# Kernel optimization log

Measured on AMD Instinct MI355X. Metric: run time of the kernel, lower is better.

Reference implementation:

```python
import jax, jax.numpy as jnp
import numpy as np

B, C_IN, IMG = 64, 3, 384
P = 16                 # patch size / conv stride
HID = 768              # hidden_size
CQ = HID // 8          # query/key channels in CrissCrossAttention
H = W = IMG // P       # 24x24 token grid
NP = H * W             # 576 patches
NEG_INF = -1e30        # finite stand-in for -inf diagonal mask (grad-safe)


def setup_inputs() -> dict:
    key = jax.random.key(0)
    ks = jax.random.split(key, 10)
    s = lambda fan_in: 1.0 / np.sqrt(fan_in)
    return {
        "x": jax.random.normal(ks[0], (B, C_IN, IMG, IMG), jnp.float32),
        "patch_w": jax.random.normal(ks[1], (HID, C_IN, P, P), jnp.float32) * s(C_IN * P * P),
        "patch_b": jax.random.normal(ks[2], (HID,), jnp.float32) * 0.02,
        "wq": jax.random.normal(ks[3], (CQ, HID), jnp.float32) * s(HID),
        "bq": jax.random.normal(ks[4], (CQ,), jnp.float32) * 0.02,
        "wk": jax.random.normal(ks[5], (CQ, HID), jnp.float32) * s(HID),
        "bk": jax.random.normal(ks[6], (CQ,), jnp.float32) * 0.02,
        "wv": jax.random.normal(ks[7], (HID, HID), jnp.float32) * s(HID),
        "bv": jax.random.normal(ks[8], (HID,), jnp.float32) * 0.02,
        "gamma": jnp.zeros((1,), jnp.float32),
        "pos_emb": jax.random.normal(ks[9], (1, NP, HID), jnp.float32) * 0.02,
    }


def criss_cross_attention(x, wq, bq, wk, bk, wv, bv, gamma):
    # x: [b, c, h, w]
    b, c, h, w = x.shape
    q = jnp.einsum('oc,bchw->bohw', wq, x) + bq[None, :, None, None]   # [b,cq,h,w]
    k = jnp.einsum('oc,bchw->bohw', wk, x) + bk[None, :, None, None]   # [b,cq,h,w]
    v = jnp.einsum('oc,bchw->bohw', wv, x) + bv[None, :, None, None]   # [b,c,h,w]

    # column (H-axis) attention energies with -inf on the diagonal (self-pair)
    energy_H = jnp.einsum('bciw,bcjw->biwj', q, k)                     # [b,h,w,h]
    eye = jnp.eye(h, dtype=bool)[:, None, :]                           # [h,1,h]
    energy_H = jnp.where(eye, NEG_INF, energy_H)
    # row (W-axis) attention energies
    energy_W = jnp.einsum('bchi,bchj->bhij', q, k)                     # [b,h,w,w]

    concate = jax.nn.softmax(jnp.concatenate([energy_H, energy_W], axis=3), axis=3)
    att_H = concate[..., :h]                                           # [b,h,w,h]
    att_W = concate[..., h:]                                           # [b,h,w,w]

    out_H = jnp.einsum('biwj,bcjw->bciw', att_H, v)                    # [b,c,h,w]
    out_W = jnp.einsum('bhij,bchj->bchi', att_W, v)                    # [b,c,h,w]
    return gamma[0] * (out_H + out_W) + x


def reference(x, patch_w, patch_b, wq, bq, wk, bk, wv, bv, gamma, pos_emb):
    # patch embedding: Conv2d(3->768, kernel=16, stride=16)
    y = jax.lax.conv_general_dilated(
        x, patch_w, window_strides=(P, P), padding='VALID',
        dimension_numbers=('NCHW', 'OIHW', 'NCHW'))
    y = y + patch_b[None, :, None, None]                               # [b,768,24,24]
    y = criss_cross_attention(y, wq, bq, wk, bk, wv, bv, gamma)
    y = y.reshape(y.shape[0], y.shape[1], -1).transpose(0, 2, 1)       # [b, 576, 768]
    emb = y + pos_emb                                                  # dropout: eval-mode identity
    return emb
```

## Files before the change

kernel.cpp:

```cpp
#include <hip/hip_runtime.h>
#include <hip/hip_bf16.h>
#include <cstdint>

#define BATCH 64
#define CIN 3
#define IMG 384
#define PATCH 16
#define HID 768
#define CQ 96
#define HW24 24
#define NP 576
#define MROWS (BATCH*NP)
#define KDIM 768
#define NVQK 1024
#define NT_K 12
#define NEGINF (-1e30f)

typedef __attribute__((ext_vector_type(8))) short s16x8;
typedef __attribute__((ext_vector_type(4))) float f32x4;

__device__ __forceinline__ float bf2f(unsigned short u) {
    union { unsigned int i; float f; } x; x.i = ((unsigned int)u) << 16; return x.f;
}
__device__ __forceinline__ unsigned short f2bf(float f) {
    union { float f; unsigned int i; } x; x.f = f;
    unsigned int r = x.i + 0x7fffu + ((x.i >> 16) & 1u);
    return (unsigned short)(r >> 16);
}
__device__ __forceinline__ unsigned int f2bf2(float a, float b) {
    union { __hip_bfloat162 h; unsigned int u; } c;
    c.h = __float22bfloat162_rn(make_float2(a, b));
    return c.u;
}

__device__ __forceinline__ void gload_lds16(const void* g, void* l) {
    __builtin_amdgcn_global_load_lds(
        (const __attribute__((address_space(1))) void*)(uintptr_t)g,
        (__attribute__((address_space(3))) void*)(uint32_t)(uintptr_t)l,
        16, 0, 0);
}

__device__ __forceinline__ size_t kp_addr(int row, int col) {
    return (((size_t)(row >> 8) * NT_K + (col >> 6)) * 256 + (row & 255)) * 64 + (col & 63);
}

__global__ void k_prep(const float* __restrict__ pw, const float* __restrict__ wq,
                       const float* __restrict__ wk, const float* __restrict__ wv,
                       const float* __restrict__ bq, const float* __restrict__ bk,
                       const float* __restrict__ bv,
                       unsigned short* __restrict__ Wp, unsigned short* __restrict__ Wvqk,
                       float* __restrict__ Bvqk) {
    int t = blockIdx.x * 256 + threadIdx.x;
    if (t < HID * HID) Wp[t] = f2bf(pw[t]);
    if (t < NVQK * HID) {
        int row = t / HID; int col = t - row * HID;
        float val = 0.f;
        if (row < 768) val = wv[t];
        else if (row < 864) val = wq[(row - 768) * HID + col];
        else if (row < 960) val = wk[(row - 864) * HID + col];
        Wvqk[t] = f2bf(val);
    }
    if (t < NVQK) {
        float v = 0.f;
        if (t < 768) v = bv[t]; else if (t < 864) v = bq[t - 768]; else if (t < 960) v = bk[t - 864];
        Bvqk[t] = v;
    }
}

__device__ __forceinline__ void stageB_half(const unsigned short* __restrict__ gmat,
        int growbase, char* ldsregion, int kcol, int rl, int sp, int ldsoff0) {
    const unsigned short* g0 = gmat + (size_t)(growbase + rl) * KDIM + kcol + sp * 8;
    gload_lds16(g0, ldsregion + ldsoff0);
    gload_lds16(g0 + (size_t)8 * KDIM, ldsregion + ldsoff0 + 1024);
}

__global__ __launch_bounds__(512, 2) void k_gemmFused(
    const float* __restrict__ x, const unsigned short* __restrict__ Bw,
    const float* __restrict__ bias, unsigned short* __restrict__ Y,
    float* __restrict__ outF, const float* __restrict__ pos,
    const float* __restrict__ gamma)
{
    extern __shared__ char smem[];
    const int tid  = threadIdx.x;
    const int lane = tid & 63;
    const int w    = tid >> 6;
    const int wm   = w >> 2;
    const int wn   = w & 3;

    const int nwg = gridDim.x;
    const int chunk = nwg >> 3;
    const int bid = blockIdx.x;
    const int bs = (bid & 7) * chunk + (bid >> 3);
    const int bx = bs / 3, by = bs - (bs / 3) * 3;
    const int blockN = by << 8;

    const int rl = (w << 4) + (lane >> 3);
    const int sp = (lane & 7) ^ (lane >> 3);
    const int ldsoff0 = (w << 11) + (lane << 4);

    const int lx   = (lane & 15) << 7;
    const int swz  = (lane & 7) << 4;
    const int cbx0 = (((lane >> 4) << 4)) ^ swz;
    const int cbx1 = (64 + ((lane >> 4) << 4)) ^ swz;

    const int rr  = tid >> 1;
    const int ch  = (tid & 1) << 5;
    const int iib = ch >> 4;
    const int grow = (bx << 8) + rr;
    const int b  = grow / NP;
    const int p  = grow - b * NP;
    const int ph = p / HW24, pw = p - ph * HW24;
    const float* xrow = x + (size_t)b * (CIN * IMG * IMG) + ph * (PATCH * IMG) + pw * PATCH;
    const int swzr  = (rr & 7) << 4;
    const int wbase = rr * 128;

    char* Acur = smem;
    char* Anxt = smem + 32768;
    char* Bcur = smem + 65536;
    char* Bnxt = smem + 98304;

    float4 ld[8];
    auto loadA = [&](int t) {
        const float* src = xrow + (t >> 2) * (IMG * IMG) + ((t & 3) * 4 + iib) * IMG;
        #pragma unroll
        for (int u = 0; u < 4; ++u) {
            const float* s2 = src + (u >> 1) * IMG + ((u & 1) << 3);
            ld[2 * u]     = *(const float4*)s2;
            ld[2 * u + 1] = *(const float4*)(s2 + 4);
        }
    };
    auto writeA = [&](char* dst) {
        #pragma unroll
        for (int u = 0; u < 4; ++u) {
            int4 pk;
            pk.x = f2bf2(ld[2 * u].x,     ld[2 * u].y);
            pk.y = f2bf2(ld[2 * u].z,     ld[2 * u].w);
            pk.z = f2bf2(ld[2 * u + 1].x, ld[2 * u + 1].y);
            pk.w = f2bf2(ld[2 * u + 1].z, ld[2 * u + 1].w);
            *reinterpret_cast<int4*>(dst + wbase + ((ch * 2 + u * 16) ^ swzr)) = pk;
        }
    };

    loadA(0);
    stageB_half(Bw, blockN,       Bcur,         0, rl, sp, ldsoff0);
    stageB_half(Bw, blockN + 128, Bcur + 16384, 0, rl, sp, ldsoff0);
    asm volatile("s_waitcnt vmcnt(0)" ::: "memory");
    __builtin_amdgcn_sched_barrier(0);
    writeA(Acur);
    asm volatile("s_waitcnt lgkmcnt(0)" ::: "memory");
    __builtin_amdgcn_sched_barrier(0);
    __builtin_amdgcn_s_barrier();

    f32x4 acc[8][4] = {};

    for (int t = 0; t < NT_K; ++t) {
        if (t + 1 < NT_K) {
            loadA(t + 1);
            stageB_half(Bw, blockN,       Bnxt,         (t + 1) << 6, rl, sp, ldsoff0);
            stageB_half(Bw, blockN + 128, Bnxt + 16384, (t + 1) << 6, rl, sp, ldsoff0);
        }
        s16x8 bfr[4][2];
        #pragma unroll
        for (int nf = 0; nf < 4; ++nf) {
            const int rb = wn * 8192 + nf * 2048 + lx;
            bfr[nf][0] = *(const s16x8*)(Bcur + rb + cbx0);
            bfr[nf][1] = *(const s16x8*)(Bcur + rb + cbx1);
        }
        #pragma unroll
        for (int half = 0; half < 2; ++half) {
            s16x8 af[4][2];
            #pragma unroll
            for (int m = 0; m < 4; ++m) {
                const int rb0 = wm * 16384 + (half * 4 + m) * 2048 + lx;
                af[m][0] = *(const s16x8*)(Acur + rb0 + cbx0);
                af[m][1] = *(const s16x8*)(Acur + rb0 + cbx1);
            }
            __builtin_amdgcn_s_setprio(1);
            #pragma unroll
            for (int kh = 0; kh < 2; ++kh)
                #pragma unroll
                for (int m = 0; m < 4; ++m)
                    #pragma unroll
                    for (int nf = 0; nf < 4; ++nf)
                        acc[half * 4 + m][nf] = __builtin_amdgcn_mfma_f32_16x16x32_bf16(
                            bfr[nf][kh], af[m][kh], acc[half * 4 + m][nf], 0, 0, 0);
            __builtin_amdgcn_s_setprio(0);
        }
        if (t + 1 < NT_K) {
            __builtin_amdgcn_sched_barrier(0);
            asm volatile("s_waitcnt vmcnt(0)" ::: "memory");
            __builtin_amdgcn_sched_barrier(0);
            writeA(Anxt);
            asm volatile("s_waitcnt lgkmcnt(0)" ::: "memory");
            __builtin_amdgcn_sched_barrier(0);
            __builtin_amdgcn_s_barrier();
            char* ta = Acur; Acur = Anxt; Anxt = ta;
            char* tb = Bcur; Bcur = Bnxt; Bnxt = tb;
        }
    }

    const int rowb = (bx << 8) + wm * 128 + (lane & 15);
    const int colb = blockN + wn * 64 + ((lane >> 4) << 2);
    const float g = gamma[0];
    if (g == 0.f) {
        #pragma unroll
        for (int mf = 0; mf < 8; ++mf) {
            const int row = rowb + mf * 16;
            const int px = row % NP;
            #pragma unroll
            for (int nf = 0; nf < 4; ++nf) {
                const int col = colb + nf * 16;
                float4 bs4 = *(const float4*)(bias + col);
                float4 pv  = *(const float4*)(pos + (size_t)px * HID + col);
                f32x4 a = acc[mf][nf];
                float4 o;
                o.x = a[0] + bs4.x + pv.x;
                o.y = a[1] + bs4.y + pv.y;
                o.z = a[2] + bs4.z + pv.z;
                o.w = a[3] + bs4.w + pv.w;
                *reinterpret_cast<float4*>(outF + (size_t)row * HID + col) = o;
            }
        }
    } else {
        #pragma unroll
        for (int mf = 0; mf < 8; ++mf) {
            const int row = rowb + mf * 16;
            #pragma unroll
            for (int nf = 0; nf < 4; ++nf) {
                const int col = colb + nf * 16;
                float4 bs4 = *(const float4*)(bias + col);
                f32x4 a = acc[mf][nf];
                ushort4 o;
                o.x = f2bf(a[0] + bs4.x);
                o.y = f2bf(a[1] + bs4.y);
                o.z = f2bf(a[2] + bs4.z);
                o.w = f2bf(a[3] + bs4.w);
                *reinterpret_cast<ushort4*>(Y + kp_addr(row, col)) = o;
            }
        }
    }
}

__device__ __forceinline__ void stageA_half(const unsigned short* __restrict__ Ap,
        size_t tilebase, int h, char* ldsregion, int rl, int sp, int ldsoff0) {
    const unsigned short* g0 = Ap + tilebase + (size_t)(h * 128 + rl) * 64 + sp * 8;
    gload_lds16(g0, ldsregion + ldsoff0);
    gload_lds16(g0 + 512, ldsregion + ldsoff0 + 1024);
}

__global__ __launch_bounds__(512, 2) void k_gemm256(
    const unsigned short* __restrict__ A, const unsigned short* __restrict__ Bw,
    const float* __restrict__ bias, unsigned short* __restrict__ C,
    const float* __restrict__ gamma, int NT)
{
    if (gamma[0] == 0.f) return;
    extern __shared__ char smem[];
    const int tid  = threadIdx.x;
    const int lane = tid & 63;
    const int w    = tid >> 6;
    const int wm   = w >> 2;
    const int wn   = w & 3;
    const int nwg = gridDim.x;
    const int chunk = nwg >> 3;
    const int bid = blockIdx.x;
    const int bs = (bid & 7) * chunk + (bid >> 3);
    const int bx = bs / NT, by = bs - (bs / NT) * NT;
    const int blockN = by << 8;
    const int rl = (w << 4) + (lane >> 3);
    const int sp = (lane & 7) ^ (lane >> 3);
    const int ldsoff0 = (w << 11) + (lane << 4);
    const int lx   = (lane & 15) << 7;
    const int swz  = (lane & 7) << 4;
    const int cbx0 = (((lane >> 4) << 4)) ^ swz;
    const int cbx1 = (64 + ((lane >> 4) << 4)) ^ swz;
    char* pa0 = smem;
    char* pa1 = smem + 32768;
    char* pa2 = smem + 65536;
    char* pb0 = smem + 98304;
    char* pb1 = smem + 131072;
    const size_t atile0 = ((size_t)bx * NT_K) << 14;

    stageB_half(Bw, blockN,       pb0,         0,  rl, sp, ldsoff0);
    stageB_half(Bw, blockN + 128, pb0 + 16384, 0,  rl, sp, ldsoff0);
    stageA_half(A, atile0,         0, pa0,         rl, sp, ldsoff0);
    stageA_half(A, atile0,         1, pa0 + 16384, rl, sp, ldsoff0);
    stageA_half(A, atile0 + 16384, 0, pa1,         rl, sp, ldsoff0);
    stageA_half(A, atile0 + 16384, 1, pa1 + 16384, rl, sp, ldsoff0);

    f32x4 acc[8][4] = {};
    asm volatile("s_waitcnt vmcnt(4)" ::: "memory");
    __builtin_amdgcn_sched_barrier(0);
    __builtin_amdgcn_s_barrier();

    for (int t = 0; t < NT_K; ++t) {
        if (t + 1 < NT_K) {
            stageB_half(Bw, blockN,       pb1,         (t + 1) << 6, rl, sp, ldsoff0);
            stageB_half(Bw, blockN + 128, pb1 + 16384, (t + 1) << 6, rl, sp, ldsoff0);
        }
        if (t + 2 < NT_K) {
            const size_t tb = atile0 + ((size_t)(t + 2) << 14);
            stageA_half(A, tb, 0, pa2,         rl, sp, ldsoff0);
            stageA_half(A, tb, 1, pa2 + 16384, rl, sp, ldsoff0);
        }
        s16x8 bfr[4][2];
        #pragma unroll
        for (int nf = 0; nf < 4; ++nf) {
            const int rb = wn * 8192 + nf * 2048 + lx;
            bfr[nf][0] = *(const s16x8*)(pb0 + rb + cbx0);
            bfr[nf][1] = *(const s16x8*)(pb0 + rb + cbx1);
        }
        #pragma unroll
        for (int half = 0; half < 2; ++half) {
            s16x8 af[4][2];
            #pragma unroll
            for (int m = 0; m < 4; ++m) {
                const int rb0 = wm * 16384 + (half * 4 + m) * 2048 + lx;
                af[m][0] = *(const s16x8*)(pa0 + rb0 + cbx0);
                af[m][1] = *(const s16x8*)(pa0 + rb0 + cbx1);
            }
            __builtin_amdgcn_s_setprio(1);
            #pragma unroll
            for (int kh = 0; kh < 2; ++kh)
                #pragma unroll
                for (int m = 0; m < 4; ++m)
                    #pragma unroll
                    for (int nf = 0; nf < 4; ++nf)
                        acc[half * 4 + m][nf] = __builtin_amdgcn_mfma_f32_16x16x32_bf16(
                            bfr[nf][kh], af[m][kh], acc[half * 4 + m][nf], 0, 0, 0);
            __builtin_amdgcn_s_setprio(0);
        }
        if (t < NT_K - 1) {
            __builtin_amdgcn_sched_barrier(0);
            if (t >= NT_K - 3) { asm volatile("s_waitcnt vmcnt(0)" ::: "memory"); }
            else               { asm volatile("s_waitcnt vmcnt(4)" ::: "memory"); }
            __builtin_amdgcn_s_barrier();
            __builtin_amdgcn_sched_barrier(0);
        }
        char* ta = pa0; pa0 = pa1; pa1 = pa2; pa2 = ta;
        char* tb = pb0; pb0 = pb1; pb1 = tb;
    }

    const int rowb = (bx << 8) + wm * 128 + (lane & 15);
    const int colb = blockN + wn * 64 + ((lane >> 4) << 2);
    #pragma unroll
    for (int mf = 0; mf < 8; ++mf) {
        const int row = rowb + mf * 16;
        #pragma unroll
        for (int nf = 0; nf < 4; ++nf) {
            const int col = colb + nf * 16;
            float4 bs4 = *(const float4*)(bias + col);
            f32x4 a = acc[mf][nf];
            ushort4 o;
            o.x = f2bf(a[0] + bs4.x);
            o.y = f2bf(a[1] + bs4.y);
            o.z = f2bf(a[2] + bs4.z);
            o.w = f2bf(a[3] + bs4.w);
            *reinterpret_cast<ushort4*>(C + (size_t)row * (NT << 8) + col) = o;
        }
    }
}

__global__ __launch_bounds__(256) void k_energyH(const unsigned short* __restrict__ VQK,
                                                 float* __restrict__ E, const float* __restrict__ gam) {
    if (gam[0] == 0.f) return;
    __shared__ float qs[24][97], ks[24][97];
    const int b = blockIdx.x / HW24, w = blockIdx.x % HW24;
    const int tid = threadIdx.x;
    for (int idx = tid; idx < 24 * 12; idx += 256) {
        int i = idx / 12, c = (idx % 12) * 8;
        size_t base = ((size_t)(b * NP + i * HW24 + w)) * NVQK + 768;
        s16x8 qv = *(const s16x8*)(VQK + base + c);
        s16x8 kv = *(const s16x8*)(VQK + base + 96 + c);
        #pragma unroll
        for (int u = 0; u < 8; u++) {
            qs[i][c + u] = bf2f((unsigned short)qv[u]);
            ks[i][c + u] = bf2f((unsigned short)kv[u]);
        }
    }
    __syncthreads();
    for (int idx = tid; idx < 576; idx += 256) {
        int i = idx / 24, j = idx - (idx / 24) * 24;
        float s = NEGINF;
        if (i != j) {
            s = 0.f;
            #pragma unroll 8
            for (int c = 0; c < 96; c++) s += qs[i][c] * ks[j][c];
        }
        E[((size_t)(b * NP + i * HW24 + w)) * 48 + j] = s;
    }
}

__global__ __launch_bounds__(256) void k_energyW(const unsigned short* __restrict__ VQK,
                                                 float* __restrict__ E, const float* __restrict__ gam) {
    if (gam[0] == 0.f) return;
    __shared__ float qs[24][97], ks[24][97], ew[24][24];
    const int b = blockIdx.x / HW24, h = blockIdx.x % HW24;
    const int tid = threadIdx.x;
    const int prow = b * NP + h * HW24;
    for (int idx = tid; idx < 24 * 12; idx += 256) {
        int i = idx / 12, c = (idx % 12) * 8;
        size_t base = ((size_t)(prow + i)) * NVQK + 768;
        s16x8 qv = *(const s16x8*)(VQK + base + c);
        s16x8 kv = *(const s16x8*)(VQK + base + 96 + c);
        #pragma unroll
        for (int u = 0; u < 8; u++) {
            qs[i][c + u] = bf2f((unsigned short)qv[u]);
            ks[i][c + u] = bf2f((unsigned short)kv[u]);
        }
    }
    __syncthreads();
    for (int idx = tid; idx < 576; idx += 256) {
        int i = idx / 24, j = idx - (idx / 24) * 24;
        float s = 0.f;
        #pragma unroll 8
        for (int c = 0; c < 96; c++) s += qs[i][c] * ks[j][c];
        ew[i][j] = s;
    }
    __syncthreads();
    if (tid < 24) {
        size_t p = prow + tid;
        float e[48];
        #pragma unroll
        for (int j = 0; j < 24; j++) e[j] = E[p * 48 + j];
        #pragma unroll
        for (int j = 0; j < 24; j++) e[24 + j] = ew[tid][j];
        float mx = NEGINF;
        #pragma unroll
        for (int j = 0; j < 48; j++) mx = fmaxf(mx, e[j]);
        float sum = 0.f;
        #pragma unroll
        for (int j = 0; j < 48; j++) { e[j] = __expf(e[j] - mx); sum += e[j]; }
        float inv = 1.f / sum;
        #pragma unroll
        for (int j = 0; j < 48; j++) E[p * 48 + j] = e[j] * inv;
    }
}

__global__ __launch_bounds__(192) void k_passH(const float* __restrict__ E,
        const unsigned short* __restrict__ VQK, const unsigned short* __restrict__ Y,
        const float* __restrict__ gamma, const float* __restrict__ pos,
        float* __restrict__ out) {
    const float g = gamma[0];
    if (g == 0.f) return;
    __shared__ float att[576];
    int bid = (blockIdx.x & 7) * 192 + (blockIdx.x >> 3);
    const int b = bid / HW24, w = bid % HW24;
    const int tid = threadIdx.x;
    for (int idx = tid; idx < 576; idx += 192) {
        int i = idx / 24, j = idx - (idx / 24) * 24;
        att[idx] = E[((size_t)(b * NP + i * HW24 + w)) * 48 + j];
    }
    __syncthreads();
    float vf[24][4];
    #pragma unroll
    for (int j = 0; j < 24; j++) {
        ushort4 vv = *(const ushort4*)(VQK + ((size_t)(b * NP + j * HW24 + w)) * NVQK + 4 * tid);
        vf[j][0] = bf2f(vv.x); vf[j][1] = bf2f(vv.y); vf[j][2] = bf2f(vv.z); vf[j][3] = bf2f(vv.w);
    }
    #pragma unroll
    for (int i = 0; i < 24; i++) {
        float a0 = 0.f, a1 = 0.f, a2 = 0.f, a3 = 0.f;
        #pragma unroll
        for (int j = 0; j < 24; j++) {
            float a = att[i * 24 + j];
            a0 += a * vf[j][0]; a1 += a * vf[j][1]; a2 += a * vf[j][2]; a3 += a * vf[j][3];
        }
        size_t p = (size_t)(b * NP + i * HW24 + w);
        ushort4 yv = *(const ushort4*)(Y + kp_addr((int)p, 4 * tid));
        float4 pv = *(const float4*)(pos + (size_t)(i * HW24 + w) * HID + 4 * tid);
        float4 o;
        o.x = g * a0 + bf2f(yv.x) + pv.x;
        o.y = g * a1 + bf2f(yv.y) + pv.y;
        o.z = g * a2 + bf2f(yv.z) + pv.z;
        o.w = g * a3 + bf2f(yv.w) + pv.w;
        *reinterpret_cast<float4*>(out + p * HID + 4 * tid) = o;
    }
}

__global__ __launch_bounds__(192) void k_passW(const float* __restrict__ E,
        const unsigned short* __restrict__ VQK, const float* __restrict__ gamma,
        float* __restrict__ out) {
    const float g = gamma[0];
    if (g == 0.f) return;
    __shared__ float att[576];
    int bid = (blockIdx.x & 7) * 192 + (blockIdx.x >> 3);
    const int b = bid / HW24, h = bid % HW24;
    const int tid = threadIdx.x;
    const int prow = b * NP + h * HW24;
    for (int idx = tid; idx < 576; idx += 192) {
        int i = idx / 24, j = idx - (idx / 24) * 24;
        att[idx] = E[((size_t)(prow + i)) * 48 + 24 + j];
    }
    __syncthreads();
    float vf[24][4];
    #pragma unroll
    for (int j = 0; j < 24; j++) {
        ushort4 vv = *(const ushort4*)(VQK + ((size_t)(prow + j)) * NVQK + 4 * tid);
        vf[j][0] = bf2f(vv.x); vf[j][1] = bf2f(vv.y); vf[j][2] = bf2f(vv.z); vf[j][3] = bf2f(vv.w);
    }
    #pragma unroll
    for (int i = 0; i < 24; i++) {
        float a0 = 0.f, a1 = 0.f, a2 = 0.f, a3 = 0.f;
        #pragma unroll
        for (int j = 0; j < 24; j++) {
            float a = att[i * 24 + j];
            a0 += a * vf[j][0]; a1 += a * vf[j][1]; a2 += a * vf[j][2]; a3 += a * vf[j][3];
        }
        size_t p = (size_t)(prow + i);
        float4 o = *reinterpret_cast<const float4*>(out + p * HID + 4 * tid);
        o.x += g * a0; o.y += g * a1; o.z += g * a2; o.w += g * a3;
        *reinterpret_cast<float4*>(out + p * HID + 4 * tid) = o;
    }
}

extern "C" void kernel_launch(void* const* d_in, const int* in_sizes, int n_in,
                              void* d_out, int out_size, void* d_ws, size_t ws_size,
                              hipStream_t stream) {
    const float* x       = (const float*)d_in[0];
    const float* patch_w = (const float*)d_in[1];
    const float* patch_b = (const float*)d_in[2];
    const float* wq      = (const float*)d_in[3];
    const float* bq      = (const float*)d_in[4];
    const float* wk      = (const float*)d_in[5];
    const float* bk      = (const float*)d_in[6];
    const float* wv      = (const float*)d_in[7];
    const float* bv      = (const float*)d_in[8];
    const float* gamma   = (const float*)d_in[9];
    const float* pos_emb = (const float*)d_in[10];
    float* out = (float*)d_out;

    hipFuncSetAttribute(reinterpret_cast<const void*>(k_gemmFused),
                        hipFuncAttributeMaxDynamicSharedMemorySize, 131072);
    hipFuncSetAttribute(reinterpret_cast<const void*>(k_gemm256),
                        hipFuncAttributeMaxDynamicSharedMemorySize, 163840);

    char* ws = (char*)d_ws;
    size_t off = 0;
    auto alloc = [&](size_t bytes) { char* pp = ws + off; off += (bytes + 255) & ~(size_t)255; return pp; };
    unsigned short* VQK = (unsigned short*)alloc((size_t)MROWS * NVQK * 2);
    unsigned short* Y   = (unsigned short*)alloc((size_t)MROWS * HID * 2);
    unsigned short* Wp  = (unsigned short*)alloc((size_t)HID * HID * 2);
    unsigned short* Wvqk= (unsigned short*)alloc((size_t)NVQK * HID * 2);
    float*          Bvqk= (float*)alloc(NVQK * 4);
    float*          E   = (float*)alloc((size_t)MROWS * 48 * 4);

    k_prep<<<dim3((NVQK * HID + 255) / 256), dim3(256), 0, stream>>>(patch_w, wq, wk, wv, bq, bk, bv, Wp, Wvqk, Bvqk);
    k_gemmFused<<<dim3((MROWS / 256) * (HID / 256)), dim3(512), 131072, stream>>>(
        x, Wp, patch_b, Y, out, pos_emb, gamma);
    k_gemm256<<<dim3((MROWS / 256) * (NVQK / 256)), dim3(512), 163840, stream>>>(
        Y, Wvqk, Bvqk, VQK, gamma, NVQK / 256);
    k_energyH<<<dim3(BATCH * HW24), dim3(256), 0, stream>>>(VQK, E, gamma);
    k_energyW<<<dim3(BATCH * HW24), dim3(256), 0, stream>>>(VQK, E, gamma);
    k_passH<<<dim3(BATCH * HW24), dim3(192), 0, stream>>>(E, VQK, Y, gamma, pos_emb, out);
    k_passW<<<dim3(BATCH * HW24), dim3(192), 0, stream>>>(E, VQK, gamma, out);
}
```

Baseline: 112.0 us.

## Deepen patch-embed GEMM pipeline to prefetch two K-tiles ahead

Converts the fused patch-embedding GEMM from double buffering to a three-stage B buffer and two register sets for A. Loads for tile t+2 are issued while tile t computes, with partial vmcnt waits, so global-memory latency is hidden further. The cost is 160KB of LDS and launch bounds lowered to one block per CU, which halves occupancy and puts more pressure on registers.

```diff
diff --git a/kernel.cpp b/kernel.cpp
--- a/kernel.cpp
+++ b/kernel.cpp
@@ -74,7 +74,7 @@
     gload_lds16(g0 + (size_t)8 * KDIM, ldsregion + ldsoff0 + 1024);
 }
 
-__global__ __launch_bounds__(512, 2) void k_gemmFused(
+__global__ __launch_bounds__(512, 1) void k_gemmFused(
     const float* __restrict__ x, const unsigned short* __restrict__ Bw,
     const float* __restrict__ bias, unsigned short* __restrict__ Y,
     float* __restrict__ outF, const float* __restrict__ pos,
@@ -114,13 +114,15 @@
     const int swzr  = (rr & 7) << 4;
     const int wbase = rr * 128;
 
-    char* Acur = smem;
-    char* Anxt = smem + 32768;
-    char* Bcur = smem + 65536;
-    char* Bnxt = smem + 98304;
-
-    float4 ld[8];
-    auto loadA = [&](int t) {
+    char* paC = smem;
+    char* paN = smem + 32768;
+    char* pb0 = smem + 65536;
+    char* pb1 = smem + 98304;
+    char* pb2 = smem + 131072;
+
+    float4 ld0[8], ld1[8];
+
+    auto loadA = [&](int t, float4 (&ld)[8]) {
         const float* src = xrow + (t >> 2) * (IMG * IMG) + ((t & 3) * 4 + iib) * IMG;
         #pragma unroll
         for (int u = 0; u < 4; ++u) {
@@ -129,7 +131,7 @@
             ld[2 * u + 1] = *(const float4*)(s2 + 4);
         }
     };
-    auto writeA = [&](char* dst) {
+    auto writeA = [&](char* dst, float4 (&ld)[8]) {
         #pragma unroll
         for (int u = 0; u < 4; ++u) {
             int4 pk;
@@ -141,30 +143,35 @@
         }
     };
 
-    loadA(0);
-    stageB_half(Bw, blockN,       Bcur,         0, rl, sp, ldsoff0);
-    stageB_half(Bw, blockN + 128, Bcur + 16384, 0, rl, sp, ldsoff0);
-    asm volatile("s_waitcnt vmcnt(0)" ::: "memory");
+    f32x4 acc[8][4] = {};
+
+    loadA(0, ld0);
+    stageB_half(Bw, blockN,       pb0,         0, rl, sp, ldsoff0);
+    stageB_half(Bw, blockN + 128, pb0 + 16384, 0, rl, sp, ldsoff0);
+    loadA(1, ld1);
+    stageB_half(Bw, blockN,       pb1,         64, rl, sp, ldsoff0);
+    stageB_half(Bw, blockN + 128, pb1 + 16384, 64, rl, sp, ldsoff0);
+    asm volatile("s_waitcnt vmcnt(16)" ::: "memory");
     __builtin_amdgcn_sched_barrier(0);
-    writeA(Acur);
+    writeA(paC, ld0);
+    asm volatile("s_waitcnt vmcnt(12)" ::: "memory");
     asm volatile("s_waitcnt lgkmcnt(0)" ::: "memory");
     __builtin_amdgcn_sched_barrier(0);
     __builtin_amdgcn_s_barrier();
 
-    f32x4 acc[8][4] = {};
-
-    for (int t = 0; t < NT_K; ++t) {
-        if (t + 1 < NT_K) {
-            loadA(t + 1);
-            stageB_half(Bw, blockN,       Bnxt,         (t + 1) << 6, rl, sp, ldsoff0);
-            stageB_half(Bw, blockN + 128, Bnxt + 16384, (t + 1) << 6, rl, sp, ldsoff0);
+    auto tileBody = [&](int t, float4 (&ldIss)[8], float4 (&ldWr)[8]) {
+        const bool issue = (t + 2 < NT_K);
+        if (issue) {
+            loadA(t + 2, ldIss);
+            stageB_half(Bw, blockN,       pb2,         (t + 2) << 6, rl, sp, ldsoff0);
+            stageB_half(Bw, blockN + 128, pb2 + 16384, (t + 2) << 6, rl, sp, ldsoff0);
         }
         s16x8 bfr[4][2];
         #pragma unroll
         for (int nf = 0; nf < 4; ++nf) {
             const int rb = wn * 8192 + nf * 2048 + lx;
-            bfr[nf][0] = *(const s16x8*)(Bcur + rb + cbx0);
-            bfr[nf][1] = *(const s16x8*)(Bcur + rb + cbx1);
+            bfr[nf][0] = *(const s16x8*)(pb0 + rb + cbx0);
+            bfr[nf][1] = *(const s16x8*)(pb0 + rb + cbx1);
         }
         #pragma unroll
         for (int half = 0; half < 2; ++half) {
@@ -172,8 +179,8 @@
             #pragma unroll
             for (int m = 0; m < 4; ++m) {
                 const int rb0 = wm * 16384 + (half * 4 + m) * 2048 + lx;
-                af[m][0] = *(const s16x8*)(Acur + rb0 + cbx0);
-                af[m][1] = *(const s16x8*)(Acur + rb0 + cbx1);
+                af[m][0] = *(const s16x8*)(paC + rb0 + cbx0);
+                af[m][1] = *(const s16x8*)(paC + rb0 + cbx1);
             }
             __builtin_amdgcn_s_setprio(1);
             #pragma unroll
@@ -186,17 +193,24 @@
                             bfr[nf][kh], af[m][kh], acc[half * 4 + m][nf], 0, 0, 0);
             __builtin_amdgcn_s_setprio(0);
         }
-        if (t + 1 < NT_K) {
+        if (t < NT_K - 1) {
             __builtin_amdgcn_sched_barrier(0);
-            asm volatile("s_waitcnt vmcnt(0)" ::: "memory");
+            if (issue) { asm volatile("s_waitcnt vmcnt(12)" ::: "memory"); }
+            else       { asm volatile("s_waitcnt vmcnt(0)"  ::: "memory"); }
             __builtin_amdgcn_sched_barrier(0);
-            writeA(Anxt);
+            writeA(paN, ldWr);
             asm volatile("s_waitcnt lgkmcnt(0)" ::: "memory");
             __builtin_amdgcn_sched_barrier(0);
             __builtin_amdgcn_s_barrier();
-            char* ta = Acur; Acur = Anxt; Anxt = ta;
-            char* tb = Bcur; Bcur = Bnxt; Bnxt = tb;
-        }
+            char* ta = paC; paC = paN; paN = ta;
+            char* tb = pb0; pb0 = pb1; pb1 = pb2; pb2 = tb;
+        }
+    };
+
+    #pragma unroll 1
+    for (int tt = 0; tt < NT_K; tt += 2) {
+        tileBody(tt,     ld0, ld1);
+        tileBody(tt + 1, ld1, ld0);
     }
 
     const int rowb = (bx << 8) + wm * 128 + (lane & 15);
@@ -530,7 +544,7 @@
     float* out = (float*)d_out;
 
     hipFuncSetAttribute(reinterpret_cast<const void*>(k_gemmFused),
-                        hipFuncAttributeMaxDynamicSharedMemorySize, 131072);
+                        hipFuncAttributeMaxDynamicSharedMemorySize, 163840);
     hipFuncSetAttribute(reinterpret_cast<const void*>(k_gemm256),
                         hipFuncAttributeMaxDynamicSharedMemorySize, 163840);
 
@@ -545,7 +559,7 @@
     float*          E   = (float*)alloc((size_t)MROWS * 48 * 4);
 
     k_prep<<<dim3((NVQK * HID + 255) / 256), dim3(256), 0, stream>>>(patch_w, wq, wk, wv, bq, bk, bv, Wp, Wvqk, Bvqk);
-    k_gemmFused<<<dim3((MROWS / 256) * (HID / 256)), dim3(512), 131072, stream>>>(
+    k_gemmFused<<<dim3((MROWS / 256) * (HID / 256)), dim3(512), 163840, stream>>>(
         x, Wp, patch_b, Y, out, pos_emb, gamma);
     k_gemm256<<<dim3((MROWS / 256) * (NVQK / 256)), dim3(512), 163840, stream>>>(
         Y, Wvqk, Bvqk, VQK, gamma, NVQK / 256);
```

New measurement: 319.8 us. 2.86x slower.

## Retile patch-embed GEMM to 128x384 blocks with narrower im2col loads

Applied to the files above, without the earlier changes.

The fused patch-embedding GEMM moves from 256x256 output tiles (3 N-blocks) to 128x384 tiles (2 N-blocks). Each warp now computes a 64x96 sub-tile, so every A fragment is reused across six B fragments. The im2col A-loader now gives each thread one float4 per row instead of two, and B staging covers three 128-row halves. Launch bounds drop to one block per CU, and the grid becomes 576 blocks instead of 432, which shifts the balance between occupancy, wave quantization and operand reuse.

```diff
diff --git a/kernel.cpp b/kernel.cpp
--- a/kernel.cpp
+++ b/kernel.cpp
@@ -74,7 +74,7 @@
     gload_lds16(g0 + (size_t)8 * KDIM, ldsregion + ldsoff0 + 1024);
 }
 
-__global__ __launch_bounds__(512, 2) void k_gemmFused(
+__global__ __launch_bounds__(512, 1) void k_gemmFused(
     const float* __restrict__ x, const unsigned short* __restrict__ Bw,
     const float* __restrict__ bias, unsigned short* __restrict__ Y,
     float* __restrict__ outF, const float* __restrict__ pos,
@@ -91,8 +91,8 @@
     const int chunk = nwg >> 3;
     const int bid = blockIdx.x;
     const int bs = (bid & 7) * chunk + (bid >> 3);
-    const int bx = bs / 3, by = bs - (bs / 3) * 3;
-    const int blockN = by << 8;
+    const int bx = bs >> 1, by = bs & 1;
+    const int blockN = by * 384;
 
     const int rl = (w << 4) + (lane >> 3);
     const int sp = (lane & 7) ^ (lane >> 3);
@@ -103,112 +103,102 @@
     const int cbx0 = (((lane >> 4) << 4)) ^ swz;
     const int cbx1 = (64 + ((lane >> 4) << 4)) ^ swz;
 
-    const int rr  = tid >> 1;
-    const int ch  = (tid & 1) << 5;
-    const int iib = ch >> 4;
-    const int grow = (bx << 8) + rr;
+    const int rr = tid >> 2;
+    const int q  = tid & 3;
+    const int grow = (bx << 7) + rr;
     const int b  = grow / NP;
     const int p  = grow - b * NP;
     const int ph = p / HW24, pw = p - ph * HW24;
-    const float* xrow = x + (size_t)b * (CIN * IMG * IMG) + ph * (PATCH * IMG) + pw * PATCH;
+    const float* xrow = x + (size_t)b * (CIN * IMG * IMG) + ph * (PATCH * IMG) + pw * PATCH + (q << 2);
     const int swzr  = (rr & 7) << 4;
     const int wbase = rr * 128;
 
-    char* Acur = smem;
-    char* Anxt = smem + 32768;
-    char* Bcur = smem + 65536;
-    char* Bnxt = smem + 98304;
-
-    float4 ld[8];
+    char* paC = smem;
+    char* paN = smem + 16384;
+    char* pbC = smem + 32768;
+    char* pbN = smem + 81920;
+
+    float4 ld[4];
     auto loadA = [&](int t) {
-        const float* src = xrow + (t >> 2) * (IMG * IMG) + ((t & 3) * 4 + iib) * IMG;
-        #pragma unroll
-        for (int u = 0; u < 4; ++u) {
-            const float* s2 = src + (u >> 1) * IMG + ((u & 1) << 3);
-            ld[2 * u]     = *(const float4*)s2;
-            ld[2 * u + 1] = *(const float4*)(s2 + 4);
-        }
+        const float* src = xrow + (t >> 2) * (IMG * IMG) + ((t & 3) << 2) * IMG;
+        #pragma unroll
+        for (int u = 0; u < 4; ++u) ld[u] = *(const float4*)(src + u * IMG);
     };
     auto writeA = [&](char* dst) {
         #pragma unroll
         for (int u = 0; u < 4; ++u) {
-            int4 pk;
-            pk.x = f2bf2(ld[2 * u].x,     ld[2 * u].y);
-            pk.y = f2bf2(ld[2 * u].z,     ld[2 * u].w);
-            pk.z = f2bf2(ld[2 * u + 1].x, ld[2 * u + 1].y);
-            pk.w = f2bf2(ld[2 * u + 1].z, ld[2 * u + 1].w);
-            *reinterpret_cast<int4*>(dst + wbase + ((ch * 2 + u * 16) ^ swzr)) = pk;
+            int2 pk;
+            pk.x = f2bf2(ld[u].x, ld[u].y);
+            pk.y = f2bf2(ld[u].z, ld[u].w);
+            *reinterpret_cast<int2*>(dst + wbase + (((u << 5) + (q << 3)) ^ swzr)) = pk;
         }
     };
+    auto stageB3 = [&](char* dst, int kcol) {
+        stageB_half(Bw, blockN,       dst,         kcol, rl, sp, ldsoff0);
+        stageB_half(Bw, blockN + 128, dst + 16384, kcol, rl, sp, ldsoff0);
+        stageB_half(Bw, blockN + 256, dst + 32768, kcol, rl, sp, ldsoff0);
+    };
+
+    f32x4 acc[4][6] = {};
 
     loadA(0);
-    stageB_half(Bw, blockN,       Bcur,         0, rl, sp, ldsoff0);
-    stageB_half(Bw, blockN + 128, Bcur + 16384, 0, rl, sp, ldsoff0);
-    asm volatile("s_waitcnt vmcnt(0)" ::: "memory");
+    stageB3(pbC, 0);
+    asm volatile("s_waitcnt vmcnt(6)" ::: "memory");
     __builtin_amdgcn_sched_barrier(0);
-    writeA(Acur);
-    asm volatile("s_waitcnt lgkmcnt(0)" ::: "memory");
+    writeA(paC);
+    asm volatile("s_waitcnt vmcnt(0) lgkmcnt(0)" ::: "memory");
     __builtin_amdgcn_sched_barrier(0);
     __builtin_amdgcn_s_barrier();
-
-    f32x4 acc[8][4] = {};
 
     for (int t = 0; t < NT_K; ++t) {
         if (t + 1 < NT_K) {
             loadA(t + 1);
-            stageB_half(Bw, blockN,       Bnxt,         (t + 1) << 6, rl, sp, ldsoff0);
-            stageB_half(Bw, blockN + 128, Bnxt + 16384, (t + 1) << 6, rl, sp, ldsoff0);
-        }
-        s16x8 bfr[4][2];
-        #pragma unroll
-        for (int nf = 0; nf < 4; ++nf) {
-            const int rb = wn * 8192 + nf * 2048 + lx;
-            bfr[nf][0] = *(const s16x8*)(Bcur + rb + cbx0);
-            bfr[nf][1] = *(const s16x8*)(Bcur + rb + cbx1);
-        }
-        #pragma unroll
-        for (int half = 0; half < 2; ++half) {
-            s16x8 af[4][2];
+            stageB3(pbN, (t + 1) << 6);
+        }
+        s16x8 af[4][2];
+        #pragma unroll
+        for (int m = 0; m < 4; ++m) {
+            const int rb0 = wm * 8192 + m * 2048 + lx;
+            af[m][0] = *(const s16x8*)(paC + rb0 + cbx0);
+            af[m][1] = *(const s16x8*)(paC + rb0 + cbx1);
+        }
+        __builtin_amdgcn_s_setprio(1);
+        #pragma unroll
+        for (int nf = 0; nf < 6; ++nf) {
+            const int rb = wn * 12288 + nf * 2048 + lx;
+            s16x8 b0 = *(const s16x8*)(pbC + rb + cbx0);
+            s16x8 b1 = *(const s16x8*)(pbC + rb + cbx1);
             #pragma unroll
-            for (int m = 0; m < 4; ++m) {
-                const int rb0 = wm * 16384 + (half * 4 + m) * 2048 + lx;
-                af[m][0] = *(const s16x8*)(Acur + rb0 + cbx0);
-                af[m][1] = *(const s16x8*)(Acur + rb0 + cbx1);
-            }
-            __builtin_amdgcn_s_setprio(1);
+            for (int m = 0; m < 4; ++m)
+                acc[m][nf] = __builtin_amdgcn_mfma_f32_16x16x32_bf16(b0, af[m][0], acc[m][nf], 0, 0, 0);
             #pragma unroll
-            for (int kh = 0; kh < 2; ++kh)
-                #pragma unroll
-                for (int m = 0; m < 4; ++m)
-                    #pragma unroll
-                    for (int nf = 0; nf < 4; ++nf)
-                        acc[half * 4 + m][nf] = __builtin_amdgcn_mfma_f32_16x16x32_bf16(
-                            bfr[nf][kh], af[m][kh], acc[half * 4 + m][nf], 0, 0, 0);
-            __builtin_amdgcn_s_setprio(0);
-        }
+            for (int m = 0; m < 4; ++m)
+                acc[m][nf] = __builtin_amdgcn_mfma_f32_16x16x32_bf16(b1, af[m][1], acc[m][nf], 0, 0, 0);
+        }
+        __builtin_amdgcn_s_setprio(0);
         if (t + 1 < NT_K) {
             __builtin_amdgcn_sched_barrier(0);
             asm volatile("s_waitcnt vmcnt(0)" ::: "memory");
             __builtin_amdgcn_sched_barrier(0);
-            writeA(Anxt);
+            writeA(paN);
             asm volatile("s_waitcnt lgkmcnt(0)" ::: "memory");
             __builtin_amdgcn_sched_barrier(0);
             __builtin_amdgcn_s_barrier();
-            char* ta = Acur; Acur = Anxt; Anxt = ta;
-            char* tb = Bcur; Bcur = Bnxt; Bnxt = tb;
-        }
-    }
-
-    const int rowb = (bx << 8) + wm * 128 + (lane & 15);
-    const int colb = blockN + wn * 64 + ((lane >> 4) << 2);
+            char* ta = paC; paC = paN; paN = ta;
+            char* tb = pbC; pbC = pbN; pbN = tb;
+        }
+    }
+
+    const int rowb = (bx << 7) + wm * 64 + (lane & 15);
+    const int colb = blockN + wn * 96 + ((lane >> 4) << 2);
     const float g = gamma[0];
     if (g == 0.f) {
         #pragma unroll
-        for (int mf = 0; mf < 8; ++mf) {
+        for (int mf = 0; mf < 4; ++mf) {
             const int row = rowb + mf * 16;
             const int px = row % NP;
             #pragma unroll
-            for (int nf = 0; nf < 4; ++nf) {
+            for (int nf = 0; nf < 6; ++nf) {
                 const int col = colb + nf * 16;
                 float4 bs4 = *(const float4*)(bias + col);
                 float4 pv  = *(const float4*)(pos + (size_t)px * HID + col);
@@ -223,10 +213,10 @@
         }
     } else {
         #pragma unroll
-        for (int mf = 0; mf < 8; ++mf) {
+        for (int mf = 0; mf < 4; ++mf) {
             const int row = rowb + mf * 16;
             #pragma unroll
-            for (int nf = 0; nf < 4; ++nf) {
+            for (int nf = 0; nf < 6; ++nf) {
                 const int col = colb + nf * 16;
                 float4 bs4 = *(const float4*)(bias + col);
                 f32x4 a = acc[mf][nf];
@@ -545,7 +535,7 @@
     float*          E   = (float*)alloc((size_t)MROWS * 48 * 4);
 
     k_prep<<<dim3((NVQK * HID + 255) / 256), dim3(256), 0, stream>>>(patch_w, wq, wk, wv, bq, bk, bv, Wp, Wvqk, Bvqk);
-    k_gemmFused<<<dim3((MROWS / 256) * (HID / 256)), dim3(512), 131072, stream>>>(
+    k_gemmFused<<<dim3((MROWS / 128) * 2), dim3(512), 131072, stream>>>(
         x, Wp, patch_b, Y, out, pos_emb, gamma);
     k_gemm256<<<dim3((MROWS / 256) * (NVQK / 256)), dim3(512), 163840, stream>>>(
         Y, Wvqk, Bvqk, VQK, gamma, NVQK / 256);
```

New measurement: 115.3 us. 2.9% more time.

## Shrink patch-embed GEMM tile to 128x128 with single LDS buffer

Applied to the files above, without the earlier changes.

Reworks the fused patch-embedding GEMM from 256x256 tiles with 512 threads and 128KB of double-buffered LDS to 128x128 tiles with 256 threads and 32KB of static single-buffered LDS. The grid grows from 432 to 1728 blocks, and A-tile global loads are prefetched two steps ahead in registers. Together these aim to raise occupancy and improve load balance across CUs. The trade-off is less data reuse per block and an extra barrier per K step, since a single LDS buffer serialises staging with compute.

```diff
diff --git a/kernel.cpp b/kernel.cpp
--- a/kernel.cpp
+++ b/kernel.cpp
@@ -74,25 +74,25 @@
     gload_lds16(g0 + (size_t)8 * KDIM, ldsregion + ldsoff0 + 1024);
 }
 
-__global__ __launch_bounds__(512, 2) void k_gemmFused(
+__global__ __launch_bounds__(256, 3) void k_gemmFused(
     const float* __restrict__ x, const unsigned short* __restrict__ Bw,
     const float* __restrict__ bias, unsigned short* __restrict__ Y,
     float* __restrict__ outF, const float* __restrict__ pos,
     const float* __restrict__ gamma)
 {
-    extern __shared__ char smem[];
+    __shared__ char smem[32768];
+    char* Abuf = smem;
+    char* Bbuf = smem + 16384;
     const int tid  = threadIdx.x;
     const int lane = tid & 63;
     const int w    = tid >> 6;
-    const int wm   = w >> 2;
-    const int wn   = w & 3;
-
-    const int nwg = gridDim.x;
-    const int chunk = nwg >> 3;
-    const int bid = blockIdx.x;
-    const int bs = (bid & 7) * chunk + (bid >> 3);
-    const int bx = bs / 3, by = bs - (bs / 3) * 3;
-    const int blockN = by << 8;
+    const int wm   = w >> 1;
+    const int wn   = w & 1;
+
+    const int chunk = gridDim.x >> 3;
+    const int bs = (blockIdx.x & 7) * chunk + (blockIdx.x >> 3);
+    const int bx = bs / 6, by = bs - (bs / 6) * 6;
+    const int blockN = by << 7;
 
     const int rl = (w << 4) + (lane >> 3);
     const int sp = (lane & 7) ^ (lane >> 3);
@@ -106,7 +106,7 @@
     const int rr  = tid >> 1;
     const int ch  = (tid & 1) << 5;
     const int iib = ch >> 4;
-    const int grow = (bx << 8) + rr;
+    const int grow = (bx << 7) + rr;
     const int b  = grow / NP;
     const int p  = grow - b * NP;
     const int ph = p / HW24, pw = p - ph * HW24;
@@ -114,11 +114,6 @@
     const int swzr  = (rr & 7) << 4;
     const int wbase = rr * 128;
 
-    char* Acur = smem;
-    char* Anxt = smem + 32768;
-    char* Bcur = smem + 65536;
-    char* Bnxt = smem + 98304;
-
     float4 ld[8];
     auto loadA = [&](int t) {
         const float* src = xrow + (t >> 2) * (IMG * IMG) + ((t & 3) * 4 + iib) * IMG;
@@ -129,7 +124,7 @@
             ld[2 * u + 1] = *(const float4*)(s2 + 4);
         }
     };
-    auto writeA = [&](char* dst) {
+    auto writeA = [&]() {
         #pragma unroll
         for (int u = 0; u < 4; ++u) {
             int4 pk;
@@ -137,74 +132,75 @@
             pk.y = f2bf2(ld[2 * u].z,     ld[2 * u].w);
             pk.z = f2bf2(ld[2 * u + 1].x, ld[2 * u + 1].y);
             pk.w = f2bf2(ld[2 * u + 1].z, ld[2 * u + 1].w);
-            *reinterpret_cast<int4*>(dst + wbase + ((ch * 2 + u * 16) ^ swzr)) = pk;
+            *reinterpret_cast<int4*>(Abuf + wbase + ((ch * 2 + u * 16) ^ swzr)) = pk;
         }
     };
+    auto stageB = [&](int kcol) {
+        const unsigned short* g0 = Bw + (size_t)(blockN + rl) * KDIM + kcol + sp * 8;
+        gload_lds16(g0,                     Bbuf + ldsoff0);
+        gload_lds16(g0 + (size_t)8 * KDIM,  Bbuf + ldsoff0 + 1024);
+        gload_lds16(g0 + (size_t)64 * KDIM, Bbuf + ldsoff0 + 8192);
+        gload_lds16(g0 + (size_t)72 * KDIM, Bbuf + ldsoff0 + 9216);
+    };
+
+    f32x4 acc[4][4] = {};
 
     loadA(0);
-    stageB_half(Bw, blockN,       Bcur,         0, rl, sp, ldsoff0);
-    stageB_half(Bw, blockN + 128, Bcur + 16384, 0, rl, sp, ldsoff0);
-    asm volatile("s_waitcnt vmcnt(0)" ::: "memory");
-    __builtin_amdgcn_sched_barrier(0);
-    writeA(Acur);
+    stageB(0);
+    writeA();
+    loadA(1);
+    asm volatile("s_waitcnt vmcnt(8)" ::: "memory");
     asm volatile("s_waitcnt lgkmcnt(0)" ::: "memory");
     __builtin_amdgcn_sched_barrier(0);
     __builtin_amdgcn_s_barrier();
 
-    f32x4 acc[8][4] = {};
-
+    #pragma unroll 1
     for (int t = 0; t < NT_K; ++t) {
-        if (t + 1 < NT_K) {
-            loadA(t + 1);
-            stageB_half(Bw, blockN,       Bnxt,         (t + 1) << 6, rl, sp, ldsoff0);
-            stageB_half(Bw, blockN + 128, Bnxt + 16384, (t + 1) << 6, rl, sp, ldsoff0);
-        }
-        s16x8 bfr[4][2];
+        s16x8 af[4][2], bf[4][2];
+        #pragma unroll
+        for (int m = 0; m < 4; ++m) {
+            const int rb0 = wm * 8192 + m * 2048 + lx;
+            af[m][0] = *(const s16x8*)(Abuf + rb0 + cbx0);
+            af[m][1] = *(const s16x8*)(Abuf + rb0 + cbx1);
+        }
         #pragma unroll
         for (int nf = 0; nf < 4; ++nf) {
             const int rb = wn * 8192 + nf * 2048 + lx;
-            bfr[nf][0] = *(const s16x8*)(Bcur + rb + cbx0);
-            bfr[nf][1] = *(const s16x8*)(Bcur + rb + cbx1);
-        }
-        #pragma unroll
-        for (int half = 0; half < 2; ++half) {
-            s16x8 af[4][2];
+            bf[nf][0] = *(const s16x8*)(Bbuf + rb + cbx0);
+            bf[nf][1] = *(const s16x8*)(Bbuf + rb + cbx1);
+        }
+        __builtin_amdgcn_s_setprio(1);
+        #pragma unroll
+        for (int kh = 0; kh < 2; ++kh)
             #pragma unroll
-            for (int m = 0; m < 4; ++m) {
-                const int rb0 = wm * 16384 + (half * 4 + m) * 2048 + lx;
-                af[m][0] = *(const s16x8*)(Acur + rb0 + cbx0);
-                af[m][1] = *(const s16x8*)(Acur + rb0 + cbx1);
+            for (int m = 0; m < 4; ++m)
+                #pragma unroll
+                for (int nf = 0; nf < 4; ++nf)
+                    acc[m][nf] = __builtin_amdgcn_mfma_f32_16x16x32_bf16(
+                        bf[nf][kh], af[m][kh], acc[m][nf], 0, 0, 0);
+        __builtin_amdgcn_s_setprio(0);
+        if (t < NT_K - 1) {
+            __builtin_amdgcn_s_barrier();
+            stageB((t + 1) << 6);
+            writeA();
+            if (t + 2 < NT_K) {
+                loadA(t + 2);
+                asm volatile("s_waitcnt vmcnt(8)" ::: "memory");
+            } else {
+                asm volatile("s_waitcnt vmcnt(0)" ::: "memory");
             }
-            __builtin_amdgcn_s_setprio(1);
-            #pragma unroll
-            for (int kh = 0; kh < 2; ++kh)
-                #pragma unroll
-                for (int m = 0; m < 4; ++m)
-                    #pragma unroll
-                    for (int nf = 0; nf < 4; ++nf)
-                        acc[half * 4 + m][nf] = __builtin_amdgcn_mfma_f32_16x16x32_bf16(
-                            bfr[nf][kh], af[m][kh], acc[half * 4 + m][nf], 0, 0, 0);
-            __builtin_amdgcn_s_setprio(0);
-        }
-        if (t + 1 < NT_K) {
-            __builtin_amdgcn_sched_barrier(0);
-            asm volatile("s_waitcnt vmcnt(0)" ::: "memory");
-            __builtin_amdgcn_sched_barrier(0);
-            writeA(Anxt);
             asm volatile("s_waitcnt lgkmcnt(0)" ::: "memory");
             __builtin_amdgcn_sched_barrier(0);
             __builtin_amdgcn_s_barrier();
-            char* ta = Acur; Acur = Anxt; Anxt = ta;
-            char* tb = Bcur; Bcur = Bnxt; Bnxt = tb;
-        }
-    }
-
-    const int rowb = (bx << 8) + wm * 128 + (lane & 15);
+        }
+    }
+
+    const int rowb = (bx << 7) + wm * 64 + (lane & 15);
     const int colb = blockN + wn * 64 + ((lane >> 4) << 2);
     const float g = gamma[0];
     if (g == 0.f) {
         #pragma unroll
-        for (int mf = 0; mf < 8; ++mf) {
+        for (int mf = 0; mf < 4; ++mf) {
             const int row = rowb + mf * 16;
             const int px = row % NP;
             #pragma unroll
@@ -223,7 +219,7 @@
         }
     } else {
         #pragma unroll
-        for (int mf = 0; mf < 8; ++mf) {
+        for (int mf = 0; mf < 4; ++mf) {
             const int row = rowb + mf * 16;
             #pragma unroll
             for (int nf = 0; nf < 4; ++nf) {
@@ -529,8 +525,6 @@
     const float* pos_emb = (const float*)d_in[10];
     float* out = (float*)d_out;
 
-    hipFuncSetAttribute(reinterpret_cast<const void*>(k_gemmFused),
-                        hipFuncAttributeMaxDynamicSharedMemorySize, 131072);
     hipFuncSetAttribute(reinterpret_cast<const void*>(k_gemm256),
                         hipFuncAttributeMaxDynamicSharedMemorySize, 163840);
 
@@ -545,7 +539,7 @@
     float*          E   = (float*)alloc((size_t)MROWS * 48 * 4);
 
     k_prep<<<dim3((NVQK * HID + 255) / 256), dim3(256), 0, stream>>>(patch_w, wq, wk, wv, bq, bk, bv, Wp, Wvqk, Bvqk);
-    k_gemmFused<<<dim3((MROWS / 256) * (HID / 256)), dim3(512), 131072, stream>>>(
+    k_gemmFused<<<dim3((MROWS / 128) * (HID / 128)), dim3(256), 0, stream>>>(
         x, Wp, patch_b, Y, out, pos_emb, gamma);
     k_gemm256<<<dim3((MROWS / 256) * (NVQK / 256)), dim3(512), 163840, stream>>>(
         Y, Wvqk, Bvqk, VQK, gamma, NVQK / 256);
```

Result: slower. 163.8 us (+46.3%).
